# Performance work log

Hardware: AMD Instinct MI355X
Metric: run time of the kernel (lower is better)

## Reference

```python
import jax, jax.numpy as jnp
import numpy as np

# Decoder (keras) config: embed_dim=128, num_heads=8, num_att_layers=3, clip=10.0
B, NQ, NC, E, H, L, D = 512, 64, 1000, 128, 8, 3, 4
HD = E // H          # head_depth = 16
CLIP = 10.0


def setup_inputs() -> dict:
    key = jax.random.key(0)
    ks = jax.random.split(key, 12)
    s = 1.0 / np.sqrt(E)

    def w(k, shape):
        return jax.random.normal(k, shape, jnp.float32) * s

    return {
        "h": jax.random.normal(ks[0], (B, NQ, E), jnp.float32),
        "c": jax.random.normal(ks[1], (B, NC, E), jnp.float32),
        "mask": jnp.zeros((B, NQ, NC + 1), bool),
        "clusters": jnp.zeros((B, D, NC), bool),
        "depot_id": 0,
        # stacked per-layer GAT (multi-head self-attention) params [L, E, E]/[L, E]
        "gat_Wq": w(ks[2], (L, E, E)), "gat_bq": jnp.zeros((L, E), jnp.float32),
        "gat_Wk": w(ks[3], (L, E, E)), "gat_bk": jnp.zeros((L, E), jnp.float32),
        "gat_Wv": w(ks[4], (L, E, E)), "gat_bv": jnp.zeros((L, E), jnp.float32),
        "gat_Wo": w(ks[5], (L, E, E)), "gat_bo": jnp.zeros((L, E), jnp.float32),
        # decoder query/key dense layers (use_bias=True)
        "Wq": w(ks[6], (E, E)), "bq": jnp.zeros((E,), jnp.float32),
        "Wk": w(ks[7], (E, E)), "bk": jnp.zeros((E,), jnp.float32),
    }


def _mha_layer(x, Wq, bq, Wk, bk, Wv, bv, Wo, bo):
    # One Graph_Attention_Module: multi-head self-attention + residual.
    Bx, N, Ex = x.shape
    q = (x @ Wq + bq).reshape(Bx, N, H, HD)
    k = (x @ Wk + bk).reshape(Bx, N, H, HD)
    v = (x @ Wv + bv).reshape(Bx, N, H, HD)
    att = jax.nn.softmax(jnp.einsum('bqhd,bkhd->bhqk', q, k) / np.sqrt(HD), axis=-1)
    o = jnp.einsum('bhqk,bkhd->bqhd', att, v).reshape(Bx, N, Ex)
    return x + o @ Wo + bo


def reference(h, c, mask, clusters, depot_id,
              gat_Wq, gat_bq, gat_Wk, gat_bk, gat_Wv, gat_bv, gat_Wo, gat_bo,
              Wq, bq, Wk, bk):
    # --- MHGAT ---
    x = h
    for i in range(L):  # small fixed layer loop
        x = _mha_layer(x, gat_Wq[i], gat_bq[i], gat_Wk[i], gat_bk[i],
                       gat_Wv[i], gat_bv[i], gat_Wo[i], gat_bo[i])
    query = x @ Wq + bq            # [B, NQ, E]
    key = c @ Wk + bk              # [B, NC, E]
    # tanh-clipped compatibility: tanh(QK^T / sqrt(head_depth)) * clip
    compat = jnp.tanh(jnp.einsum('bqe,bke->bqk', query, key) / np.sqrt(HD)) * CLIP
    compat = jnp.where(mask[:, :, 1:], -jnp.inf, compat)   # drop depot column of mask

    # --- select_cust (vectorized: masked log_softmax + argmax per batch) ---
    compts = jnp.mean(compat, axis=1)          # [B, NC]
    clust = clusters[:, depot_id, :]           # [B, NC]
    tt = jnp.where(clust, -jnp.inf, compts)
    log_p = jax.nn.log_softmax(tt, axis=-1)
    action = jnp.argmax(log_p, axis=-1)[:, None]  # [B, 1]
    return action, compat
```

## Files before the change

### kernel.cpp

```cpp
#include <hip/hip_runtime.h>
#include <math.h>

#define NB   512
#define NQ   64
#define NCC  1000
#define EE   128
#define HH   8
#define HDD  16
#define NL   3
#define DD   4
#define KP   136
#define XP   136
#define VP   72

typedef __bf16 bf16x8 __attribute__((ext_vector_type(8)));
typedef unsigned short u16x8 __attribute__((ext_vector_type(8)));
typedef unsigned short u16x4 __attribute__((ext_vector_type(4)));
typedef unsigned int   u32x4 __attribute__((ext_vector_type(4)));
typedef float f32x4  __attribute__((ext_vector_type(4)));
typedef float f32x16 __attribute__((ext_vector_type(16)));

__device__ __forceinline__ unsigned short f2bf(float x) {
  union { float f; unsigned u; } v; v.f = x;
  unsigned r = (v.u + 0x7fffu + ((v.u >> 16) & 1u)) >> 16;
  return (unsigned short)r;
}
__device__ __forceinline__ float bf2f(unsigned short h) {
  union { unsigned u; float f; } v; v.u = ((unsigned)h) << 16;
  return v.f;
}
__device__ __forceinline__ bf16x8 ld8(const unsigned short* p) {
  return __builtin_bit_cast(bf16x8, *(const u16x8*)p);
}

__global__ __launch_bounds__(256) void wprep_kernel(
    const float* __restrict__ gWq, const float* __restrict__ gWk,
    const float* __restrict__ gWv, const float* __restrict__ gWo,
    const float* __restrict__ Wq,  const float* __restrict__ Wk,
    unsigned short* __restrict__ gwt_hi, unsigned short* __restrict__ gwt_lo)
{
  const int idx = blockIdx.x * 256 + threadIdx.x;
  const int m = idx >> 14;
  const int r = idx & 16383;
  const int k = r >> 7, n = r & 127;
  const float* src;
  if (m < 12) {
    const int l = m >> 2, w = m & 3;
    src = (w == 0 ? gWq : w == 1 ? gWk : w == 2 ? gWv : gWo) + l * 16384;
  } else if (m == 12) src = Wq;
  else                src = Wk;
  const float v = src[k * EE + n];
  const unsigned short h = f2bf(v);
  gwt_hi[(size_t)m * 16384 + n * EE + k] = h;
  gwt_lo[(size_t)m * 16384 + n * EE + k] = f2bf(v - bf2f(h));
}

__global__ __launch_bounds__(512, 1) void gat_query_mfma(
    const float* __restrict__ hin,
    const unsigned short* __restrict__ gwt_hi,
    const unsigned short* __restrict__ gwt_lo,
    const float* __restrict__ gbq, const float* __restrict__ gbk,
    const float* __restrict__ gbv, const float* __restrict__ gbo,
    const float* __restrict__ bq,
    float* __restrict__ query)
{
  __shared__ unsigned short XH[64 * XP], XL[64 * XP];
  __shared__ unsigned short QH[64 * XP], QL[64 * XP];
  __shared__ unsigned short KH[64 * XP], KL[64 * XP];
  __shared__ unsigned short VTH[128 * VP], VTL[128 * VP];

  const int b    = blockIdx.x;
  const int tid  = threadIdx.x;
  const int wid  = tid >> 6;
  const int lane = tid & 63;
  const int l15  = lane & 15;
  const int quad = lane >> 4;
  const int col  = lane & 31;
  const int hi32 = lane >> 5;

  for (int idx = tid; idx < NQ * EE; idx += 512) {
    const float v = hin[(size_t)b * NQ * EE + idx];
    const int r = idx >> 7, c = idx & 127;
    const unsigned short h = f2bf(v);
    XH[r * XP + c] = h;
    XL[r * XP + c] = f2bf(v - bf2f(h));
  }
  __syncthreads();

  const int mt = wid >> 1, nh = wid & 1;
  const int r0 = mt * 16;

  for (int l = 0; l < NL; ++l) {
    {
      bf16x8 axh[4], axl[4];
      #pragma unroll
      for (int k4 = 0; k4 < 4; ++k4) {
        axh[k4] = ld8(&XH[(r0 + l15) * XP + k4 * 32 + quad * 8]);
        axl[k4] = ld8(&XL[(r0 + l15) * XP + k4 * 32 + quad * 8]);
      }
      #pragma unroll
      for (int m = 0; m < 3; ++m) {
        const unsigned short* WH = gwt_hi + (size_t)(l * 4 + m) * 16384;
        const unsigned short* WL = gwt_lo + (size_t)(l * 4 + m) * 16384;
        const float* bias = (m == 0 ? gbq : (m == 1 ? gbk : gbv)) + l * EE;
        #pragma unroll
        for (int ntl = 0; ntl < 4; ++ntl) {
          const int n = (nh * 4 + ntl) * 16 + l15;
          f32x4 acc = (f32x4){0.f, 0.f, 0.f, 0.f};
          #pragma unroll
          for (int k4 = 0; k4 < 4; ++k4) {
            const int k0 = k4 * 32 + quad * 8;
            const bf16x8 bh = ld8(&WH[n * EE + k0]);
            const bf16x8 bl = ld8(&WL[n * EE + k0]);
            acc = __builtin_amdgcn_mfma_f32_16x16x32_bf16(axh[k4], bh, acc, 0, 0, 0);
            acc = __builtin_amdgcn_mfma_f32_16x16x32_bf16(axh[k4], bl, acc, 0, 0, 0);
            acc = __builtin_amdgcn_mfma_f32_16x16x32_bf16(axl[k4], bh, acc, 0, 0, 0);
          }
          const float bv = bias[n];
          if (m == 2) {
            u16x4 hv, lv;
            #pragma unroll
            for (int r = 0; r < 4; ++r) {
              const float v = acc[r] + bv;
              const unsigned short h = f2bf(v);
              hv[r] = h;
              lv[r] = f2bf(v - bf2f(h));
            }
            *(u16x4*)&VTH[n * VP + r0 + quad * 4] = hv;
            *(u16x4*)&VTL[n * VP + r0 + quad * 4] = lv;
          } else {
            unsigned short* DH = m ? KH : QH;
            unsigned short* DL = m ? KL : QL;
            #pragma unroll
            for (int r = 0; r < 4; ++r) {
              const int crow = r0 + quad * 4 + r;
              const float v = acc[r] + bv;
              const unsigned short h = f2bf(v);
              DH[crow * XP + n] = h;
              DL[crow * XP + n] = f2bf(v - bf2f(h));
            }
          }
        }
      }
    }
    __syncthreads();

    {
      const int hwid = wid;
      const int hb = hwid * 16 + hi32 * 8;
      bf16x8 akh[2], akl[2], qbh[2], qbl[2];
      #pragma unroll
      for (int t = 0; t < 2; ++t) {
        akh[t] = ld8(&KH[(t * 32 + col) * XP + hb]);
        akl[t] = ld8(&KL[(t * 32 + col) * XP + hb]);
        qbh[t] = ld8(&QH[(t * 32 + col) * XP + hb]);
        qbl[t] = ld8(&QL[(t * 32 + col) * XP + hb]);
      }

      bf16x8 pah[2][4], pal[2][4];
      #pragma unroll
      for (int qt = 0; qt < 2; ++qt) {
        f32x16 sAcc[2];
        #pragma unroll
        for (int kt = 0; kt < 2; ++kt) {
          #pragma unroll
          for (int i = 0; i < 16; ++i) sAcc[kt][i] = 0.f;
          sAcc[kt] = __builtin_amdgcn_mfma_f32_32x32x16_bf16(akh[kt], qbh[qt], sAcc[kt], 0, 0, 0);
          sAcc[kt] = __builtin_amdgcn_mfma_f32_32x32x16_bf16(akh[kt], qbl[qt], sAcc[kt], 0, 0, 0);
          sAcc[kt] = __builtin_amdgcn_mfma_f32_32x32x16_bf16(akl[kt], qbh[qt], sAcc[kt], 0, 0, 0);
        }
        float p[2][16];
        float mx = -INFINITY;
        #pragma unroll
        for (int kt = 0; kt < 2; ++kt)
          #pragma unroll
          for (int r = 0; r < 16; ++r) {
            p[kt][r] = sAcc[kt][r] * 0.25f;
            mx = fmaxf(mx, p[kt][r]);
          }
        mx = fmaxf(mx, __shfl_xor(mx, 32));
        float sum = 0.f;
        #pragma unroll
        for (int kt = 0; kt < 2; ++kt)
          #pragma unroll
          for (int r = 0; r < 16; ++r) {
            p[kt][r] = exp2f((p[kt][r] - mx) * 1.4426950408889634f);
            sum += p[kt][r];
          }
        sum += __shfl_xor(sum, 32);
        const float inv = 1.f / sum;

        unsigned pkh[2][8], pkl[2][8], swh[2][8], swl[2][8];
        #pragma unroll
        for (int kt = 0; kt < 2; ++kt)
          #pragma unroll
          for (int w = 0; w < 8; ++w) {
            const float v0 = p[kt][w * 2]     * inv;
            const float v1 = p[kt][w * 2 + 1] * inv;
            const unsigned short h0 = f2bf(v0);
            const unsigned short l0 = f2bf(v0 - bf2f(h0));
            const unsigned short h1 = f2bf(v1);
            const unsigned short l1 = f2bf(v1 - bf2f(h1));
            pkh[kt][w] = (unsigned)h0 | ((unsigned)h1 << 16);
            pkl[kt][w] = (unsigned)l0 | ((unsigned)l1 << 16);
            swh[kt][w] = (unsigned)__shfl_xor((int)pkh[kt][w], 32);
            swl[kt][w] = (unsigned)__shfl_xor((int)pkl[kt][w], 32);
          }
        const bool top = (hi32 != 0);
        #pragma unroll
        for (int ks = 0; ks < 4; ++ks) {
          const int kt = ks >> 1, hf = ks & 1;
          u32x4 wh, wl;
          wh[0] = top ? swh[kt][4 * hf + 2] : pkh[kt][4 * hf + 0];
          wh[1] = top ? swh[kt][4 * hf + 3] : pkh[kt][4 * hf + 1];
          wh[2] = top ? pkh[kt][4 * hf + 2] : swh[kt][4 * hf + 0];
          wh[3] = top ? pkh[kt][4 * hf + 3] : swh[kt][4 * hf + 1];
          wl[0] = top ? swl[kt][4 * hf + 2] : pkl[kt][4 * hf + 0];
          wl[1] = top ? swl[kt][4 * hf + 3] : pkl[kt][4 * hf + 1];
          wl[2] = top ? pkl[kt][4 * hf + 2] : swl[kt][4 * hf + 0];
          wl[3] = top ? pkl[kt][4 * hf + 3] : swl[kt][4 * hf + 1];
          pah[qt][ks] = __builtin_bit_cast(bf16x8, wh);
          pal[qt][ks] = __builtin_bit_cast(bf16x8, wl);
        }
      }

      bf16x8 bvh[4], bvl[4];
      const int vrow = hwid * 16 + (col & 15);
      #pragma unroll
      for (int ks = 0; ks < 4; ++ks) {
        bvh[ks] = ld8(&VTH[vrow * VP + ks * 16 + hi32 * 8]);
        bvl[ks] = ld8(&VTL[vrow * VP + ks * 16 + hi32 * 8]);
      }
      f32x16 accO[2];
      #pragma unroll
      for (int qt = 0; qt < 2; ++qt) {
        #pragma unroll
        for (int i = 0; i < 16; ++i) accO[qt][i] = 0.f;
        #pragma unroll
        for (int ks = 0; ks < 4; ++ks) {
          accO[qt] = __builtin_amdgcn_mfma_f32_32x32x16_bf16(pah[qt][ks], bvh[ks], accO[qt], 0, 0, 0);
          accO[qt] = __builtin_amdgcn_mfma_f32_32x32x16_bf16(pah[qt][ks], bvl[ks], accO[qt], 0, 0, 0);
          accO[qt] = __builtin_amdgcn_mfma_f32_32x32x16_bf16(pal[qt][ks], bvh[ks], accO[qt], 0, 0, 0);
        }
      }
      if (col < 16) {
        #pragma unroll
        for (int qt = 0; qt < 2; ++qt)
          #pragma unroll
          for (int r = 0; r < 16; ++r) {
            const int qrow = qt * 32 + (r & 3) + 8 * (r >> 2) + 4 * hi32;
            const float v = accO[qt][r];
            const unsigned short h = f2bf(v);
            KH[qrow * XP + hwid * 16 + col] = h;
            KL[qrow * XP + hwid * 16 + col] = f2bf(v - bf2f(h));
          }
      }
    }
    __syncthreads();

    {
      bf16x8 aoh[4], aol[4];
      #pragma unroll
      for (int k4 = 0; k4 < 4; ++k4) {
        aoh[k4] = ld8(&KH[(r0 + l15) * XP + k4 * 32 + quad * 8]);
        aol[k4] = ld8(&KL[(r0 + l15) * XP + k4 * 32 + quad * 8]);
      }
      const unsigned short* WH = gwt_hi + (size_t)(l * 4 + 3) * 16384;
      const unsigned short* WL = gwt_lo + (size_t)(l * 4 + 3) * 16384;
      #pragma unroll
      for (int ntl = 0; ntl < 4; ++ntl) {
        const int n = (nh * 4 + ntl) * 16 + l15;
        f32x4 acc = (f32x4){0.f, 0.f, 0.f, 0.f};
        #pragma unroll
        for (int k4 = 0; k4 < 4; ++k4) {
          const int k0 = k4 * 32 + quad * 8;
          const bf16x8 bh = ld8(&WH[n * EE + k0]);
          const bf16x8 bl = ld8(&WL[n * EE + k0]);
          acc = __builtin_amdgcn_mfma_f32_16x16x32_bf16(aoh[k4], bh, acc, 0, 0, 0);
          acc = __builtin_amdgcn_mfma_f32_16x16x32_bf16(aoh[k4], bl, acc, 0, 0, 0);
          acc = __builtin_amdgcn_mfma_f32_16x16x32_bf16(aol[k4], bh, acc, 0, 0, 0);
        }
        const float bv = gbo[l * EE + n];
        #pragma unroll
        for (int r = 0; r < 4; ++r) {
          const int crow = r0 + quad * 4 + r;
          const float xo = bf2f(XH[crow * XP + n]) + bf2f(XL[crow * XP + n]);
          const float v = xo + acc[r] + bv;
          const unsigned short h = f2bf(v);
          XH[crow * XP + n] = h;
          XL[crow * XP + n] = f2bf(v - bf2f(h));
        }
      }
    }
    __syncthreads();
  }

  {
    bf16x8 axh[4], axl[4];
    #pragma unroll
    for (int k4 = 0; k4 < 4; ++k4) {
      axh[k4] = ld8(&XH[(r0 + l15) * XP + k4 * 32 + quad * 8]);
      axl[k4] = ld8(&XL[(r0 + l15) * XP + k4 * 32 + quad * 8]);
    }
    const unsigned short* WH = gwt_hi + (size_t)12 * 16384;
    const unsigned short* WL = gwt_lo + (size_t)12 * 16384;
    #pragma unroll
    for (int ntl = 0; ntl < 4; ++ntl) {
      const int n = (nh * 4 + ntl) * 16 + l15;
      f32x4 acc = (f32x4){0.f, 0.f, 0.f, 0.f};
      #pragma unroll
      for (int k4 = 0; k4 < 4; ++k4) {
        const int k0 = k4 * 32 + quad * 8;
        const bf16x8 bh = ld8(&WH[n * EE + k0]);
        const bf16x8 bl = ld8(&WL[n * EE + k0]);
        acc = __builtin_amdgcn_mfma_f32_16x16x32_bf16(axh[k4], bh, acc, 0, 0, 0);
        acc = __builtin_amdgcn_mfma_f32_16x16x32_bf16(axh[k4], bl, acc, 0, 0, 0);
        acc = __builtin_amdgcn_mfma_f32_16x16x32_bf16(axl[k4], bh, acc, 0, 0, 0);
      }
      const float bv = bq[n];
      #pragma unroll
      for (int r = 0; r < 4; ++r) {
        const int crow = r0 + quad * 4 + r;
        query[((size_t)b * NQ + crow) * EE + n] = acc[r] + bv;
      }
    }
  }
}

__global__ __launch_bounds__(256, 2) void compat_mfma_kernel(
    const float* __restrict__ cin,
    const float* __restrict__ query,
    const unsigned char* __restrict__ mask,
    const unsigned short* __restrict__ wkt_hi,
    const unsigned short* __restrict__ wkt_lo,
    const float* __restrict__ bk,
    float* __restrict__ compat_out,
    float* __restrict__ compts)
{
  __shared__ unsigned short Khi[128 * KP];
  __shared__ unsigned short Klo[128 * KP];
  __shared__ float colsum[128];

  const int ch   = blockIdx.x;
  const int b    = blockIdx.y;
  const int tid  = threadIdx.x;
  const int wave = tid >> 6;
  const int lane = tid & 63;
  const int l15  = lane & 15;
  const int quad = lane >> 4;

  if (tid < 128) colsum[tid] = 0.f;

  {
    f32x4 acc[2][8];
    #pragma unroll
    for (int mt = 0; mt < 2; ++mt)
      #pragma unroll
      for (int nt = 0; nt < 8; ++nt)
        acc[mt][nt] = (f32x4){0.f, 0.f, 0.f, 0.f};

    #pragma unroll
    for (int k4 = 0; k4 < 4; ++k4) {
      const int k0 = k4 * 32 + quad * 8;
      bf16x8 ahi[2], alo[2];
      #pragma unroll
      for (int mt = 0; mt < 2; ++mt) {
        int grow = ch * 128 + (wave * 2 + mt) * 16 + l15;
        if (grow > NCC - 1) grow = NCC - 1;
        const float* src = &cin[((size_t)b * NCC + grow) * EE + k0];
        const float4 x0 = *(const float4*)&src[0];
        const float4 x1 = *(const float4*)&src[4];
        float xv[8] = {x0.x, x0.y, x0.z, x0.w, x1.x, x1.y, x1.z, x1.w};
        u16x8 h, lo;
        #pragma unroll
        for (int j = 0; j < 8; ++j) {
          unsigned short hb = f2bf(xv[j]);
          h[j] = hb;
          lo[j] = f2bf(xv[j] - bf2f(hb));
        }
        ahi[mt] = __builtin_bit_cast(bf16x8, h);
        alo[mt] = __builtin_bit_cast(bf16x8, lo);
      }
      #pragma unroll
      for (int nt = 0; nt < 8; ++nt) {
        const int n = nt * 16 + l15;
        const bf16x8 bhi = __builtin_bit_cast(bf16x8, *(const u16x8*)&wkt_hi[n * EE + k0]);
        const bf16x8 blo = __builtin_bit_cast(bf16x8, *(const u16x8*)&wkt_lo[n * EE + k0]);
        #pragma unroll
        for (int mt = 0; mt < 2; ++mt) {
          acc[mt][nt] = __builtin_amdgcn_mfma_f32_16x16x32_bf16(ahi[mt], bhi, acc[mt][nt], 0, 0, 0);
          acc[mt][nt] = __builtin_amdgcn_mfma_f32_16x16x32_bf16(ahi[mt], blo, acc[mt][nt], 0, 0, 0);
          acc[mt][nt] = __builtin_amdgcn_mfma_f32_16x16x32_bf16(alo[mt], bhi, acc[mt][nt], 0, 0, 0);
        }
      }
    }

    #pragma unroll
    for (int nt = 0; nt < 8; ++nt) {
      const int n = nt * 16 + l15;
      const float bkv = bk[n];
      #pragma unroll
      for (int mt = 0; mt < 2; ++mt) {
        #pragma unroll
        for (int r = 0; r < 4; ++r) {
          const int crow = (wave * 2 + mt) * 16 + quad * 4 + r;
          const float v = acc[mt][nt][r] + bkv;
          const unsigned short hb = f2bf(v);
          Khi[crow * KP + n] = hb;
          Klo[crow * KP + n] = f2bf(v - bf2f(hb));
        }
      }
    }
  }
  __syncthreads();

  {
    bf16x8 qhi[4], qlo[4];
    #pragma unroll
    for (int k4 = 0; k4 < 4; ++k4) {
      const float* src = &query[((size_t)b * NQ + wave * 16 + l15) * EE + k4 * 32 + quad * 8];
      const float4 x0 = *(const float4*)&src[0];
      const float4 x1 = *(const float4*)&src[4];
      float xv[8] = {x0.x, x0.y, x0.z, x0.w, x1.x, x1.y, x1.z, x1.w};
      u16x8 h, lo;
      #pragma unroll
      for (int j = 0; j < 8; ++j) {
        unsigned short hb = f2bf(xv[j]);
        h[j] = hb;
        lo[j] = f2bf(xv[j] - bf2f(hb));
      }
      qhi[k4] = __builtin_bit_cast(bf16x8, h);
      qlo[k4] = __builtin_bit_cast(bf16x8, lo);
    }

    f32x4 acc[8];
    #pragma unroll
    for (int nt = 0; nt < 8; ++nt) acc[nt] = (f32x4){0.f, 0.f, 0.f, 0.f};

    #pragma unroll
    for (int k4 = 0; k4 < 4; ++k4) {
      const int k0 = k4 * 32 + quad * 8;
      #pragma unroll
      for (int nt = 0; nt < 8; ++nt) {
        const int crow = nt * 16 + l15;
        const bf16x8 khf = __builtin_bit_cast(bf16x8, *(const u16x8*)&Khi[crow * KP + k0]);
        const bf16x8 klf = __builtin_bit_cast(bf16x8, *(const u16x8*)&Klo[crow * KP + k0]);
        acc[nt] = __builtin_amdgcn_mfma_f32_16x16x32_bf16(qhi[k4], khf, acc[nt], 0, 0, 0);
        acc[nt] = __builtin_amdgcn_mfma_f32_16x16x32_bf16(qhi[k4], klf, acc[nt], 0, 0, 0);
        acc[nt] = __builtin_amdgcn_mfma_f32_16x16x32_bf16(qlo[k4], khf, acc[nt], 0, 0, 0);
      }
    }

    #pragma unroll
    for (int nt = 0; nt < 8; ++nt) {
      const int jloc  = nt * 16 + l15;
      const int jglob = ch * 128 + jloc;
      const bool jok  = (jglob < NCC);
      float s4 = 0.f;
      #pragma unroll
      for (int r = 0; r < 4; ++r) {
        const int q = wave * 16 + quad * 4 + r;
        float v = tanhf(acc[nt][r] * 0.25f) * 10.f;
        if (jok) {
          if (mask[((size_t)b * NQ + q) * (NCC + 1) + 1 + jglob]) v = -INFINITY;
          compat_out[((size_t)b * NQ + q) * NCC + jglob] = v;
        }
        s4 += v;
      }
      s4 += __shfl_xor(s4, 16);
      s4 += __shfl_xor(s4, 32);
      if (lane < 16 && jok) atomicAdd(&colsum[jloc], s4);
    }
  }
  __syncthreads();

  if (tid < 128) {
    const int jglob = ch * 128 + tid;
    if (jglob < NCC)
      compts[(size_t)b * 1024 + jglob] = colsum[tid] * (1.0f / (float)NQ);
  }
}

__global__ __launch_bounds__(256) void argmax_kernel(
    const float* __restrict__ compts,
    const unsigned char* __restrict__ clusters,
    const int* __restrict__ depot_id,
    float* __restrict__ out)
{
  __shared__ float redv[256];
  __shared__ int   redi[256];
  const int b   = blockIdx.x;
  const int tid = threadIdx.x;
  const int dep = depot_id[0];
  float bestv = -INFINITY;
  int   besti = 0x7fffffff;
  for (int j = tid; j < NCC; j += 256) {
    float t = compts[(size_t)b * 1024 + j];
    if (clusters[((size_t)b * DD + dep) * NCC + j]) t = -INFINITY;
    if (t > bestv || (t == bestv && j < besti)) { bestv = t; besti = j; }
  }
  redv[tid] = bestv; redi[tid] = besti;
  __syncthreads();
  if (tid == 0) {
    float bv = redv[0]; int bi = redi[0];
    for (int t = 1; t < 256; ++t) {
      if (redv[t] > bv || (redv[t] == bv && redi[t] < bi)) {
        bv = redv[t]; bi = redi[t];
      }
    }
    out[b] = (float)bi;
  }
}

extern "C" void kernel_launch(void* const* d_in, const int* in_sizes, int n_in,
                              void* d_out, int out_size, void* d_ws, size_t ws_size,
                              hipStream_t stream) {
  const float* hin      = (const float*)d_in[0];
  const float* cin      = (const float*)d_in[1];
  const unsigned char* mask     = (const unsigned char*)d_in[2];
  const unsigned char* clusters = (const unsigned char*)d_in[3];
  const int*   depot    = (const int*)d_in[4];
  const float* gWq = (const float*)d_in[5];
  const float* gbq = (const float*)d_in[6];
  const float* gWk = (const float*)d_in[7];
  const float* gbk = (const float*)d_in[8];
  const float* gWv = (const float*)d_in[9];
  const float* gbv = (const float*)d_in[10];
  const float* gWo = (const float*)d_in[11];
  const float* gbo = (const float*)d_in[12];
  const float* Wq  = (const float*)d_in[13];
  const float* bq  = (const float*)d_in[14];
  const float* Wk  = (const float*)d_in[15];
  const float* bk  = (const float*)d_in[16];
  float* out   = (float*)d_out;
  float* compat_out = out + NB;

  float*          query  = (float*)d_ws;
  float*          compts = (float*)((char*)d_ws + (size_t)NB * NQ * EE * 4);
  unsigned short* gwt_hi = (unsigned short*)((char*)compts + (size_t)NB * 1024 * 4);
  unsigned short* gwt_lo = gwt_hi + (size_t)14 * 16384;
  unsigned short* wkt_hi = gwt_hi + (size_t)13 * 16384;
  unsigned short* wkt_lo = gwt_lo + (size_t)13 * 16384;

  wprep_kernel<<<896, 256, 0, stream>>>(gWq, gWk, gWv, gWo, Wq, Wk, gwt_hi, gwt_lo);
  gat_query_mfma<<<NB, 512, 0, stream>>>(hin, gwt_hi, gwt_lo,
                                         gbq, gbk, gbv, gbo, bq, query);
  compat_mfma_kernel<<<dim3(8, NB), 256, 0, stream>>>(
      cin, query, mask, wkt_hi, wkt_lo, bk, compat_out, compts);
  argmax_kernel<<<NB, 256, 0, stream>>>(compts, clusters, depot, out);
}
```

Baseline: 938.3 us.

## Halve compat chunk to 64 columns, raise occupancy, use fast tanh

The compat kernel now handles 64 customer columns per block instead of 128, so the grid doubles and the shared-memory K tile halves. The launch bound rises to 4 blocks per SM. The K projection is restructured to load all c inputs up front, then loop over output tiles with a single accumulator, which cuts register pressure. tanhf is replaced by an exp/rcp formulation that costs less per element but is slightly less accurate. The trade-off is that the query rows are loaded and split into hi/lo parts twice as often, since each block now covers fewer columns.

```diff
diff --git a/kernel.cpp b/kernel.cpp
--- a/kernel.cpp
+++ b/kernel.cpp
@@ -10,6 +10,7 @@
 #define NL   3
 #define DD   4
 #define KP   136
+#define CCH  64
 #define XP   136
 #define VP   72
 
@@ -31,6 +32,10 @@
 }
 __device__ __forceinline__ bf16x8 ld8(const unsigned short* p) {
   return __builtin_bit_cast(bf16x8, *(const u16x8*)p);
+}
+__device__ __forceinline__ float tanh10_q(float s) {
+  const float e = __expf(s * 0.5f);
+  return 10.f - 20.f * __builtin_amdgcn_rcpf(e + 1.f);
 }
 
 __global__ __launch_bounds__(256) void wprep_kernel(
@@ -327,7 +332,7 @@
   }
 }
 
-__global__ __launch_bounds__(256, 2) void compat_mfma_kernel(
+__global__ __launch_bounds__(256, 4) void compat_mfma_kernel(
     const float* __restrict__ cin,
     const float* __restrict__ query,
     const unsigned char* __restrict__ mask,
@@ -337,9 +342,9 @@
     float* __restrict__ compat_out,
     float* __restrict__ compts)
 {
-  __shared__ unsigned short Khi[128 * KP];
-  __shared__ unsigned short Klo[128 * KP];
-  __shared__ float colsum[128];
+  __shared__ unsigned short Khi[CCH * KP];
+  __shared__ unsigned short Klo[CCH * KP];
+  __shared__ float colsum[CCH];
 
   const int ch   = blockIdx.x;
   const int b    = blockIdx.y;
@@ -349,66 +354,55 @@
   const int l15  = lane & 15;
   const int quad = lane >> 4;
 
-  if (tid < 128) colsum[tid] = 0.f;
+  if (tid < CCH) colsum[tid] = 0.f;
 
   {
-    f32x4 acc[2][8];
-    #pragma unroll
-    for (int mt = 0; mt < 2; ++mt)
-      #pragma unroll
-      for (int nt = 0; nt < 8; ++nt)
-        acc[mt][nt] = (f32x4){0.f, 0.f, 0.f, 0.f};
-
+    float xv[4][8];
+    {
+      int grow = ch * CCH + wave * 16 + l15;
+      if (grow > NCC - 1) grow = NCC - 1;
+      const float* srow = &cin[((size_t)b * NCC + grow) * EE + quad * 8];
+      #pragma unroll
+      for (int k4 = 0; k4 < 4; ++k4) {
+        *(float4*)&xv[k4][0] = *(const float4*)&srow[k4 * 32 + 0];
+        *(float4*)&xv[k4][4] = *(const float4*)&srow[k4 * 32 + 4];
+      }
+    }
+    bf16x8 ahi[4], alo[4];
     #pragma unroll
     for (int k4 = 0; k4 < 4; ++k4) {
-      const int k0 = k4 * 32 + quad * 8;
-      bf16x8 ahi[2], alo[2];
-      #pragma unroll
-      for (int mt = 0; mt < 2; ++mt) {
-        int grow = ch * 128 + (wave * 2 + mt) * 16 + l15;
-        if (grow > NCC - 1) grow = NCC - 1;
-        const float* src = &cin[((size_t)b * NCC + grow) * EE + k0];
-        const float4 x0 = *(const float4*)&src[0];
-        const float4 x1 = *(const float4*)&src[4];
-        float xv[8] = {x0.x, x0.y, x0.z, x0.w, x1.x, x1.y, x1.z, x1.w};
-        u16x8 h, lo;
-        #pragma unroll
-        for (int j = 0; j < 8; ++j) {
-          unsigned short hb = f2bf(xv[j]);
-          h[j] = hb;
-          lo[j] = f2bf(xv[j] - bf2f(hb));
-        }
-        ahi[mt] = __builtin_bit_cast(bf16x8, h);
-        alo[mt] = __builtin_bit_cast(bf16x8, lo);
-      }
-      #pragma unroll
-      for (int nt = 0; nt < 8; ++nt) {
-        const int n = nt * 16 + l15;
+      u16x8 h, lo;
+      #pragma unroll
+      for (int j = 0; j < 8; ++j) {
+        unsigned short hb = f2bf(xv[k4][j]);
+        h[j] = hb;
+        lo[j] = f2bf(xv[k4][j] - bf2f(hb));
+      }
+      ahi[k4] = __builtin_bit_cast(bf16x8, h);
+      alo[k4] = __builtin_bit_cast(bf16x8, lo);
+    }
+
+    #pragma unroll
+    for (int nt = 0; nt < 8; ++nt) {
+      const int n = nt * 16 + l15;
+      f32x4 acc = (f32x4){0.f, 0.f, 0.f, 0.f};
+      #pragma unroll
+      for (int k4 = 0; k4 < 4; ++k4) {
+        const int k0 = k4 * 32 + quad * 8;
         const bf16x8 bhi = __builtin_bit_cast(bf16x8, *(const u16x8*)&wkt_hi[n * EE + k0]);
         const bf16x8 blo = __builtin_bit_cast(bf16x8, *(const u16x8*)&wkt_lo[n * EE + k0]);
-        #pragma unroll
-        for (int mt = 0; mt < 2; ++mt) {
-          acc[mt][nt] = __builtin_amdgcn_mfma_f32_16x16x32_bf16(ahi[mt], bhi, acc[mt][nt], 0, 0, 0);
-          acc[mt][nt] = __builtin_amdgcn_mfma_f32_16x16x32_bf16(ahi[mt], blo, acc[mt][nt], 0, 0, 0);
-          acc[mt][nt] = __builtin_amdgcn_mfma_f32_16x16x32_bf16(alo[mt], bhi, acc[mt][nt], 0, 0, 0);
-        }
-      }
-    }
-
-    #pragma unroll
-    for (int nt = 0; nt < 8; ++nt) {
-      const int n = nt * 16 + l15;
+        acc = __builtin_amdgcn_mfma_f32_16x16x32_bf16(ahi[k4], bhi, acc, 0, 0, 0);
+        acc = __builtin_amdgcn_mfma_f32_16x16x32_bf16(ahi[k4], blo, acc, 0, 0, 0);
+        acc = __builtin_amdgcn_mfma_f32_16x16x32_bf16(alo[k4], bhi, acc, 0, 0, 0);
+      }
       const float bkv = bk[n];
       #pragma unroll
-      for (int mt = 0; mt < 2; ++mt) {
-        #pragma unroll
-        for (int r = 0; r < 4; ++r) {
-          const int crow = (wave * 2 + mt) * 16 + quad * 4 + r;
-          const float v = acc[mt][nt][r] + bkv;
-          const unsigned short hb = f2bf(v);
-          Khi[crow * KP + n] = hb;
-          Klo[crow * KP + n] = f2bf(v - bf2f(hb));
-        }
+      for (int r = 0; r < 4; ++r) {
+        const int crow = wave * 16 + quad * 4 + r;
+        const float v = acc[r] + bkv;
+        const unsigned short hb = f2bf(v);
+        Khi[crow * KP + n] = hb;
+        Klo[crow * KP + n] = f2bf(v - bf2f(hb));
       }
     }
   }
@@ -421,27 +415,27 @@
       const float* src = &query[((size_t)b * NQ + wave * 16 + l15) * EE + k4 * 32 + quad * 8];
       const float4 x0 = *(const float4*)&src[0];
       const float4 x1 = *(const float4*)&src[4];
-      float xv[8] = {x0.x, x0.y, x0.z, x0.w, x1.x, x1.y, x1.z, x1.w};
+      float xq[8] = {x0.x, x0.y, x0.z, x0.w, x1.x, x1.y, x1.z, x1.w};
       u16x8 h, lo;
       #pragma unroll
       for (int j = 0; j < 8; ++j) {
-        unsigned short hb = f2bf(xv[j]);
+        unsigned short hb = f2bf(xq[j]);
         h[j] = hb;
-        lo[j] = f2bf(xv[j] - bf2f(hb));
+        lo[j] = f2bf(xq[j] - bf2f(hb));
       }
       qhi[k4] = __builtin_bit_cast(bf16x8, h);
       qlo[k4] = __builtin_bit_cast(bf16x8, lo);
     }
 
-    f32x4 acc[8];
-    #pragma unroll
-    for (int nt = 0; nt < 8; ++nt) acc[nt] = (f32x4){0.f, 0.f, 0.f, 0.f};
+    f32x4 acc[4];
+    #pragma unroll
+    for (int nt = 0; nt < 4; ++nt) acc[nt] = (f32x4){0.f, 0.f, 0.f, 0.f};
 
     #pragma unroll
     for (int k4 = 0; k4 < 4; ++k4) {
       const int k0 = k4 * 32 + quad * 8;
       #pragma unroll
-      for (int nt = 0; nt < 8; ++nt) {
+      for (int nt = 0; nt < 4; ++nt) {
         const int crow = nt * 16 + l15;
         const bf16x8 khf = __builtin_bit_cast(bf16x8, *(const u16x8*)&Khi[crow * KP + k0]);
         const bf16x8 klf = __builtin_bit_cast(bf16x8, *(const u16x8*)&Klo[crow * KP + k0]);
@@ -452,15 +446,15 @@
     }
 
     #pragma unroll
-    for (int nt = 0; nt < 8; ++nt) {
+    for (int nt = 0; nt < 4; ++nt) {
       const int jloc  = nt * 16 + l15;
-      const int jglob = ch * 128 + jloc;
+      const int jglob = ch * CCH + jloc;
       const bool jok  = (jglob < NCC);
       float s4 = 0.f;
       #pragma unroll
       for (int r = 0; r < 4; ++r) {
         const int q = wave * 16 + quad * 4 + r;
-        float v = tanhf(acc[nt][r] * 0.25f) * 10.f;
+        float v = tanh10_q(acc[nt][r]);
         if (jok) {
           if (mask[((size_t)b * NQ + q) * (NCC + 1) + 1 + jglob]) v = -INFINITY;
           compat_out[((size_t)b * NQ + q) * NCC + jglob] = v;
@@ -474,8 +468,8 @@
   }
   __syncthreads();
 
-  if (tid < 128) {
-    const int jglob = ch * 128 + tid;
+  if (tid < CCH) {
+    const int jglob = ch * CCH + tid;
     if (jglob < NCC)
       compts[(size_t)b * 1024 + jglob] = colsum[tid] * (1.0f / (float)NQ);
   }
@@ -545,7 +539,7 @@
   wprep_kernel<<<896, 256, 0, stream>>>(gWq, gWk, gWv, gWo, Wq, Wk, gwt_hi, gwt_lo);
   gat_query_mfma<<<NB, 512, 0, stream>>>(hin, gwt_hi, gwt_lo,
                                          gbq, gbk, gbv, gbo, bq, query);
-  compat_mfma_kernel<<<dim3(8, NB), 256, 0, stream>>>(
+  compat_mfma_kernel<<<dim3(16, NB), 256, 0, stream>>>(
       cin, query, mask, wkt_hi, wkt_lo, bk, compat_out, compts);
   argmax_kernel<<<NB, 256, 0, stream>>>(compts, clusters, depot, out);
 }
```

Result: slower. 959.9 us (+2.3%).
